# Performance work log

Measured on AMD Instinct MI355X. Metric: run time of the kernel, lower is better.

Reference implementation:

```python
import jax, jax.numpy as jnp
import numpy as np

S, D_MODEL, D_INTERNAL = 4096, 2048, 512


def setup_inputs() -> dict:
    key = jax.random.key(0)
    ks = jax.random.split(key, 11)
    sc_in = 1.0 / np.sqrt(D_MODEL)
    return {
        "input_vecs": jax.random.normal(ks[0], (S, D_MODEL), jnp.float32),
        "qw": jax.random.normal(ks[1], (D_INTERNAL, D_MODEL), jnp.float32) * sc_in,
        "qb": jax.random.normal(ks[2], (D_INTERNAL,), jnp.float32) * 0.01,
        "kw": jax.random.normal(ks[3], (D_INTERNAL, D_MODEL), jnp.float32) * sc_in,
        "kb": jax.random.normal(ks[4], (D_INTERNAL,), jnp.float32) * 0.01,
        "vw": jax.random.normal(ks[5], (D_MODEL, D_MODEL), jnp.float32) * sc_in,
        "vb": jax.random.normal(ks[6], (D_MODEL,), jnp.float32) * 0.01,
        "w1": jax.random.normal(ks[7], (D_MODEL, D_MODEL), jnp.float32) * sc_in,
        "b1": jax.random.normal(ks[8], (D_MODEL,), jnp.float32) * 0.01,
        "w2": jax.random.normal(ks[9], (D_MODEL, D_MODEL), jnp.float32) * sc_in,
        "b2": jax.random.normal(ks[10], (D_MODEL,), jnp.float32) * 0.01,
    }


def reference(input_vecs, qw, qb, kw, kb, vw, vb, w1, b1, w2, b2):
    # torch nn.Linear: y = x @ W.T + b
    q = input_vecs @ qw.T + qb              # [S, d_internal]
    k = input_vecs @ kw.T + kb              # [S, d_internal]
    v = input_vecs @ vw.T + vb              # [S, d_model]
    scale = 1.0 / jnp.sqrt(jnp.float32(D_INTERNAL))
    attn = jax.nn.softmax((q @ k.T) * scale, axis=-1)  # [S, S]
    h = attn @ v                            # [S, d_model]
    x_residual = h + input_vecs
    x = jax.nn.relu(x_residual @ w1.T + b1)
    x = x @ w2.T + b2
    hidden = x + x_residual
    return hidden, k, v
```

## Files before the change

kernel.cpp:

```cpp
#include <hip/hip_runtime.h>
#include <cstdint>
#include <cstddef>


typedef __attribute__((ext_vector_type(8))) short short8;
typedef __attribute__((ext_vector_type(4))) float f32x4;

typedef __attribute__((address_space(3))) void lds_void;
typedef __attribute__((address_space(1))) void g_void;

#define SEQ    4096
#define DMODEL 2048
#define DINT   512

#define MEMF() asm volatile("" ::: "memory")
#define BARRIER() do { MEMF(); __builtin_amdgcn_s_barrier(); MEMF(); } while (0)
#define VMCNT6() asm volatile("s_waitcnt vmcnt(6)" ::: "memory")
#define VMCNT0() asm volatile("s_waitcnt vmcnt(0)" ::: "memory")
#define LGKM0()  asm volatile("s_waitcnt lgkmcnt(0)" ::: "memory")

__device__ __forceinline__ unsigned short f2bf(float f) {
  union { float f; unsigned int u; } a;
  a.f = f;
  unsigned int u = a.u;
  u += 0x7fffu + ((u >> 16) & 1u);
  return (unsigned short)(u >> 16);
}

__global__ __launch_bounds__(256) void cast_bf16_kernel(
    const float* __restrict__ in, unsigned short* __restrict__ out, int n4) {
  int i = blockIdx.x * 256 + threadIdx.x;
  if (i >= n4) return;
  float4 v = ((const float4*)in)[i];
  ushort4 o;
  o.x = f2bf(v.x); o.y = f2bf(v.y); o.z = f2bf(v.z); o.w = f2bf(v.w);
  ((ushort4*)out)[i] = o;
}

__global__ __launch_bounds__(256) void transpose_bf16_kernel(
    const unsigned short* __restrict__ in, unsigned short* __restrict__ out,
    int R, int C) {
  __shared__ unsigned short tile[64][65];
  const int tx = threadIdx.x & 63;
  const int ty = threadIdx.x >> 6;
  const int r0 = blockIdx.x * 64;
  const int c0 = blockIdx.y * 64;
#pragma unroll
  for (int i = 0; i < 64; i += 4)
    tile[ty + i][tx] = in[(size_t)(r0 + ty + i) * C + c0 + tx];
  __syncthreads();
#pragma unroll
  for (int i = 0; i < 64; i += 4)
    out[(size_t)(c0 + ty + i) * R + r0 + tx] = tile[tx][ty + i];
}

__global__ __launch_bounds__(256)
void gemm_qkv_kernel(const unsigned short* __restrict__ A,
                     const unsigned short* __restrict__ W,
                     int M, int N, int K,
                     const float* __restrict__ qb,
                     const float* __restrict__ kb,
                     const float* __restrict__ vb,
                     float* __restrict__ outK,
                     float* __restrict__ outV,
                     unsigned short* __restrict__ Qb,
                     unsigned short* __restrict__ Kb,
                     unsigned short* __restrict__ Vb)
{
  __shared__ __align__(16) unsigned short As[2][128][32];
  __shared__ __align__(16) unsigned short Bs[2][128][32];

  const int tid  = threadIdx.x;
  const int lane = tid & 63;
  const int wave = tid >> 6;
  const int wr   = wave >> 1;
  const int wc   = wave & 1;
  const int brow = blockIdx.x * 128;
  const int bcol = blockIdx.y * 128;
  const int lr   = lane & 15;
  const int kg   = lane >> 4;

  const int srow  = tid >> 2;
  const int scol  = (tid & 3) * 8;
  const int wbase = wave * 16;
  const unsigned short* Ab = A + (size_t)(brow + srow) * K + scol;
  const unsigned short* Bb = W + (size_t)(bcol + srow) * K + scol;

  f32x4 acc[4][4];
#pragma unroll
  for (int i = 0; i < 4; i++)
#pragma unroll
    for (int j = 0; j < 4; j++) acc[i][j] = (f32x4){0.f, 0.f, 0.f, 0.f};

  auto stage = [&](int d, int k0) {
#pragma unroll
    for (int j = 0; j < 2; ++j) {
      __builtin_amdgcn_global_load_lds((const g_void*)(Ab + (size_t)(j * 64) * K + k0),
                                       (lds_void*)&As[d][j * 64 + wbase][0], 16, 0, 0);
      __builtin_amdgcn_global_load_lds((const g_void*)(Bb + (size_t)(j * 64) * K + k0),
                                       (lds_void*)&Bs[d][j * 64 + wbase][0], 16, 0, 0);
    }
  };

  auto compute = [&](int d) {
    short8 aF[4], bF[4];
#pragma unroll
    for (int mi = 0; mi < 4; ++mi)
      aF[mi] = *(const short8*)&As[d][wr * 64 + mi * 16 + lr][kg * 8];
#pragma unroll
    for (int ni = 0; ni < 4; ++ni)
      bF[ni] = *(const short8*)&Bs[d][wc * 64 + ni * 16 + lr][kg * 8];
#pragma unroll
    for (int mi = 0; mi < 4; ++mi)
#pragma unroll
      for (int ni = 0; ni < 4; ++ni)
        acc[mi][ni] = __builtin_amdgcn_mfma_f32_16x16x32_bf16(
            aF[mi], bF[ni], acc[mi][ni], 0, 0, 0);
  };

  stage(0, 0);
  __syncthreads();
  int c = 0;
  const int NT = K >> 5;
  for (int t = 0; t < NT; ++t) {
    if (t + 1 < NT) stage(c ^ 1, (t + 1) << 5);
    compute(c);
    __syncthreads();
    c ^= 1;
  }

#pragma unroll
  for (int mi = 0; mi < 4; mi++) {
#pragma unroll
    for (int ni = 0; ni < 4; ni++) {
#pragma unroll
      for (int r = 0; r < 4; r++) {
        const int row = brow + wr * 64 + mi * 16 + kg * 4 + r;
        const int col = bcol + wc * 64 + ni * 16 + lr;
        float v = acc[mi][ni][r];
        if (col < 512) {
          v += qb[col];
          Qb[(size_t)row * 512 + col] = f2bf(v);
        } else if (col < 1024) {
          const int c2 = col - 512;
          v += kb[c2];
          outK[(size_t)row * 512 + c2] = v;
          Kb[(size_t)row * 512 + c2] = f2bf(v);
        } else {
          const int c2 = col - 1024;
          v += vb[c2];
          outV[(size_t)row * 2048 + c2] = v;
          Vb[(size_t)row * 2048 + c2] = f2bf(v);
        }
      }
    }
  }
}

__global__ __launch_bounds__(512, 2)
void gemm256_kernel(const unsigned short* __restrict__ A,
                    const unsigned short* __restrict__ B,
                    int M, int N, int K,
                    const float* __restrict__ bias,
                    const float* __restrict__ resid,
                    float scale, int relu,
                    float* __restrict__ outF,
                    unsigned short* __restrict__ outB)
{
  __shared__ __align__(16) unsigned short lds[2][2][2][128][64];

  const int tid  = threadIdx.x;
  const int lane = tid & 63;
  const int wave = tid >> 6;
  const int wm   = wave >> 2;
  const int wn   = wave & 3;
  const int lr   = lane & 15;
  const int kg   = lane >> 4;
  const int brow = blockIdx.x * 256;
  const int bcol = blockIdx.y * 256;

  const int srow = tid >> 3;
  const int ssw  = ((tid & 7) * 8) ^ ((srow & 7) << 3);
  const unsigned short* Asrc = A + (size_t)(brow + srow) * K + ssw;
  const unsigned short* Bsrc = B + (size_t)(bcol + srow) * K + ssw;

  char* lbase = (char*)&lds[0][0][0][0][0];
  const int woff = wave * 1024;

  f32x4 acc[8][4];
#pragma unroll
  for (int i = 0; i < 8; ++i)
#pragma unroll
    for (int j = 0; j < 4; ++j) acc[i][j] = (f32x4){0.f, 0.f, 0.f, 0.f};

  const int NT = K >> 6;

  auto SA = [&](int d, int h, int q, int tl) {
    __builtin_amdgcn_global_load_lds(
        (const g_void*)(Asrc + (size_t)(h * 128 + q * 64) * K + tl * 64),
        (lds_void*)(lbase + d * 32768 + h * 16384 + q * 8192 + woff), 16, 0, 0);
  };
  auto SB = [&](int d, int h, int q, int tl) {
    __builtin_amdgcn_global_load_lds(
        (const g_void*)(Bsrc + (size_t)(h * 128 + q * 64) * K + tl * 64),
        (lds_void*)(lbase + 65536 + d * 32768 + h * 16384 + q * 8192 + woff), 16, 0, 0);
  };

  auto LDA = [&](short8* a, int d, int mh, int ks) {
    const char* reg = lbase + d * 32768 + wm * 16384;
    const int ke = (ks * 32 + kg * 8) ^ ((lr & 7) << 3);
#pragma unroll
    for (int i = 0; i < 4; ++i) {
      const int row = (mh * 4 + i) * 16 + lr;
      a[i] = *(const short8*)(reg + row * 128 + ke * 2);
    }
  };
  auto LDB = [&](short8* b, int d, int ks) {
    const char* reg = lbase + 65536 + d * 32768 + (wn >> 1) * 16384;
    const int ke = (ks * 32 + kg * 8) ^ ((lr & 7) << 3);
#pragma unroll
    for (int n = 0; n < 4; ++n) {
      const int row = (wn & 1) * 64 + n * 16 + lr;
      b[n] = *(const short8*)(reg + row * 128 + ke * 2);
    }
  };

  auto MM = [&](int mh, short8* a, short8* b) {
    __builtin_amdgcn_s_setprio(1);
#pragma unroll
    for (int i = 0; i < 4; ++i)
#pragma unroll
      for (int n = 0; n < 4; ++n)
        acc[mh * 4 + i][n] = __builtin_amdgcn_mfma_f32_16x16x32_bf16(
            a[i], b[n], acc[mh * 4 + i][n], 0, 0, 0);
    __builtin_amdgcn_s_setprio(0);
  };

  SA(0, 0, 0, 0); SA(0, 0, 1, 0); SA(0, 1, 0, 0); SA(0, 1, 1, 0);
  SB(0, 0, 0, 0); SB(0, 0, 1, 0); SB(0, 1, 0, 0); SB(0, 1, 1, 0);
  SB(1, 0, 0, 1); SB(1, 0, 1, 1); SA(1, 0, 0, 1);
  SB(1, 1, 0, 1); SB(1, 1, 1, 1); SA(1, 1, 0, 1);
  VMCNT6();
  BARRIER();

  short8 aT[4], bF0[4], bF1[4];
  for (int t = 0; t < NT; ++t) {
    const int buf = t & 1, nb = buf ^ 1;
    const int t1 = (t + 1 < NT) ? t + 1 : NT - 1;
    const int t2 = (t + 2 < NT) ? t + 2 : NT - 1;

    LDA(aT, buf, 0, 0); LDB(bF0, buf, 0);
    SA(nb, 0, 1, t1); SA(nb, 1, 1, t1);
    BARRIER(); MM(0, aT, bF0); BARRIER();

    LDA(aT, buf, 0, 1); LDB(bF1, buf, 1);
    BARRIER(); MM(0, aT, bF1); BARRIER();

    LDA(aT, buf, 1, 0);
    SB(buf, 0, 0, t2); SB(buf, 0, 1, t2); SA(buf, 0, 0, t2);
    BARRIER(); MM(1, aT, bF0); BARRIER();

    LDA(aT, buf, 1, 1);
    SB(buf, 1, 0, t2); SB(buf, 1, 1, t2); SA(buf, 1, 0, t2);
    BARRIER(); MM(1, aT, bF1);
    VMCNT6();
    BARRIER();
  }
  VMCNT0();

#pragma unroll
  for (int mi = 0; mi < 8; ++mi) {
#pragma unroll
    for (int ni = 0; ni < 4; ++ni) {
#pragma unroll
      for (int r = 0; r < 4; ++r) {
        const int row = brow + wm * 128 + mi * 16 + kg * 4 + r;
        const int col = bcol + wn * 64 + ni * 16 + lr;
        float v = acc[mi][ni][r] * scale;
        if (bias)  v += bias[col];
        if (resid) v += resid[(size_t)row * N + col];
        if (relu)  v = fmaxf(v, 0.0f);
        if (outF)  outF[(size_t)row * N + col] = v;
        if (outB)  outB[(size_t)row * N + col] = f2bf(v);
      }
    }
  }
}

__global__ __launch_bounds__(512, 2)
void gemm256x128_kernel(const unsigned short* __restrict__ A,
                        const unsigned short* __restrict__ B,
                        int M, int N, int K,
                        const float* __restrict__ bias,
                        const float* __restrict__ resid,
                        float scale, int relu,
                        float* __restrict__ outF,
                        unsigned short* __restrict__ outB)
{
  __shared__ __align__(16) unsigned short lds[49152];

  const int tid  = threadIdx.x;
  const int lane = tid & 63;
  const int wave = tid >> 6;
  const int wm   = wave >> 1;
  const int wn   = wave & 1;
  const int lr   = lane & 15;
  const int kg   = lane >> 4;
  const int brow = blockIdx.x * 256;
  const int bcol = blockIdx.y * 128;

  const int srow = tid >> 3;
  const int ssw  = ((tid & 7) * 8) ^ ((srow & 7) << 3);
  const unsigned short* Asrc = A + (size_t)(brow + srow) * K + ssw;
  const unsigned short* Bsrc = B + (size_t)(bcol + srow) * K + ssw;

  char* lbase = (char*)&lds[0];
  const int woff = wave * 1024;

  f32x4 acc[4][4];
#pragma unroll
  for (int i = 0; i < 4; ++i)
#pragma unroll
    for (int j = 0; j < 4; ++j) acc[i][j] = (f32x4){0.f, 0.f, 0.f, 0.f};

  const int NT = K >> 6;

  auto STAGE = [&](int d, int tl) {
#pragma unroll
    for (int r = 0; r < 4; ++r)
      __builtin_amdgcn_global_load_lds(
          (const g_void*)(Asrc + (size_t)(r * 64) * K + tl * 64),
          (lds_void*)(lbase + d * 32768 + r * 8192 + woff), 16, 0, 0);
#pragma unroll
    for (int r = 0; r < 2; ++r)
      __builtin_amdgcn_global_load_lds(
          (const g_void*)(Bsrc + (size_t)(r * 64) * K + tl * 64),
          (lds_void*)(lbase + 65536 + d * 16384 + r * 8192 + woff), 16, 0, 0);
  };

  auto RD = [&](short8* a, short8* b, int d) {
#pragma unroll
    for (int ks = 0; ks < 2; ++ks) {
      const int ke = (ks * 32 + kg * 8) ^ ((lr & 7) << 3);
      const char* ra = lbase + d * 32768;
      const char* rb = lbase + 65536 + d * 16384;
#pragma unroll
      for (int mi = 0; mi < 4; ++mi)
        a[ks * 4 + mi] = *(const short8*)(ra + (wm * 64 + mi * 16 + lr) * 128 + ke * 2);
#pragma unroll
      for (int n = 0; n < 4; ++n)
        b[ks * 4 + n] = *(const short8*)(rb + (wn * 64 + n * 16 + lr) * 128 + ke * 2);
    }
  };

  auto MMALL = [&](short8* a, short8* b) {
    __builtin_amdgcn_s_setprio(1);
#pragma unroll
    for (int ks = 0; ks < 2; ++ks)
#pragma unroll
      for (int mi = 0; mi < 4; ++mi)
#pragma unroll
        for (int n = 0; n < 4; ++n)
          acc[mi][n] = __builtin_amdgcn_mfma_f32_16x16x32_bf16(
              a[ks * 4 + mi], b[ks * 4 + n], acc[mi][n], 0, 0, 0);
    __builtin_amdgcn_s_setprio(0);
  };

  STAGE(0, 0);
  STAGE(1, 1);
  VMCNT0();
  BARRIER();
  short8 aE[8], bE[8], aO[8], bO[8];
  RD(aE, bE, 0);
  LGKM0();

  for (int t = 0; t < NT; t += 2) {
    VMCNT0();
    BARRIER();
    { const int t2 = (t + 2 < NT) ? t + 2 : NT - 1; STAGE(0, t2); }
    RD(aO, bO, 1);
    MMALL(aE, bE);
    LGKM0();
    VMCNT0();
    BARRIER();
    { const int t3 = (t + 3 < NT) ? t + 3 : NT - 1; STAGE(1, t3); }
    RD(aE, bE, 0);
    MMALL(aO, bO);
    LGKM0();
  }
  VMCNT0();

#pragma unroll
  for (int mi = 0; mi < 4; ++mi) {
#pragma unroll
    for (int ni = 0; ni < 4; ++ni) {
#pragma unroll
      for (int r = 0; r < 4; ++r) {
        const int row = brow + wm * 64 + mi * 16 + kg * 4 + r;
        const int col = bcol + wn * 64 + ni * 16 + lr;
        float v = acc[mi][ni][r] * scale;
        if (bias)  v += bias[col];
        if (resid) v += resid[(size_t)row * N + col];
        if (relu)  v = fmaxf(v, 0.0f);
        if (outF)  outF[(size_t)row * N + col] = v;
        if (outB)  outB[(size_t)row * N + col] = f2bf(v);
      }
    }
  }
}

__global__ __launch_bounds__(256) void softmax_kernel(
    const float* __restrict__ Sc, unsigned short* __restrict__ P) {
  __shared__ float redm[4];
  __shared__ float reds[4];
  const int tid = threadIdx.x;
  const int row = blockIdx.x;
  const float* src = Sc + (size_t)row * SEQ;

  float4 f0 = *(const float4*)(src + tid * 4);
  float4 f1 = *(const float4*)(src + tid * 4 + 1024);
  float4 f2 = *(const float4*)(src + tid * 4 + 2048);
  float4 f3 = *(const float4*)(src + tid * 4 + 3072);

  float lmax = fmaxf(fmaxf(fmaxf(f0.x, f0.y), fmaxf(f0.z, f0.w)),
                     fmaxf(fmaxf(f1.x, f1.y), fmaxf(f1.z, f1.w)));
  lmax = fmaxf(lmax, fmaxf(fmaxf(f2.x, f2.y), fmaxf(f2.z, f2.w)));
  lmax = fmaxf(lmax, fmaxf(fmaxf(f3.x, f3.y), fmaxf(f3.z, f3.w)));
#pragma unroll
  for (int off = 32; off > 0; off >>= 1)
    lmax = fmaxf(lmax, __shfl_xor(lmax, off, 64));
  if ((tid & 63) == 0) redm[tid >> 6] = lmax;
  __syncthreads();
  const float m = fmaxf(fmaxf(redm[0], redm[1]), fmaxf(redm[2], redm[3]));

  f0.x = __expf(f0.x - m); f0.y = __expf(f0.y - m);
  f0.z = __expf(f0.z - m); f0.w = __expf(f0.w - m);
  f1.x = __expf(f1.x - m); f1.y = __expf(f1.y - m);
  f1.z = __expf(f1.z - m); f1.w = __expf(f1.w - m);
  f2.x = __expf(f2.x - m); f2.y = __expf(f2.y - m);
  f2.z = __expf(f2.z - m); f2.w = __expf(f2.w - m);
  f3.x = __expf(f3.x - m); f3.y = __expf(f3.y - m);
  f3.z = __expf(f3.z - m); f3.w = __expf(f3.w - m);

  float lsum = (f0.x + f0.y + f0.z + f0.w) + (f1.x + f1.y + f1.z + f1.w) +
               (f2.x + f2.y + f2.z + f2.w) + (f3.x + f3.y + f3.z + f3.w);
#pragma unroll
  for (int off = 32; off > 0; off >>= 1)
    lsum += __shfl_xor(lsum, off, 64);
  if ((tid & 63) == 0) reds[tid >> 6] = lsum;
  __syncthreads();
  const float inv = 1.0f / (reds[0] + reds[1] + reds[2] + reds[3]);

  unsigned short* dst = P + (size_t)row * SEQ;
  ushort4 o0 = { f2bf(f0.x * inv), f2bf(f0.y * inv), f2bf(f0.z * inv), f2bf(f0.w * inv) };
  ushort4 o1 = { f2bf(f1.x * inv), f2bf(f1.y * inv), f2bf(f1.z * inv), f2bf(f1.w * inv) };
  ushort4 o2 = { f2bf(f2.x * inv), f2bf(f2.y * inv), f2bf(f2.z * inv), f2bf(f2.w * inv) };
  ushort4 o3 = { f2bf(f3.x * inv), f2bf(f3.y * inv), f2bf(f3.z * inv), f2bf(f3.w * inv) };
  *(ushort4*)(dst + tid * 4)        = o0;
  *(ushort4*)(dst + tid * 4 + 1024) = o1;
  *(ushort4*)(dst + tid * 4 + 2048) = o2;
  *(ushort4*)(dst + tid * 4 + 3072) = o3;
}

extern "C" void kernel_launch(void* const* d_in, const int* in_sizes, int n_in,
                              void* d_out, int out_size, void* d_ws, size_t ws_size,
                              hipStream_t stream) {
  const float* x  = (const float*)d_in[0];
  const float* qw = (const float*)d_in[1];
  const float* qb = (const float*)d_in[2];
  const float* kw = (const float*)d_in[3];
  const float* kb = (const float*)d_in[4];
  const float* vw = (const float*)d_in[5];
  const float* vb = (const float*)d_in[6];
  const float* w1 = (const float*)d_in[7];
  const float* b1 = (const float*)d_in[8];
  const float* w2 = (const float*)d_in[9];
  const float* b2 = (const float*)d_in[10];
  float* out = (float*)d_out;
  char* ws = (char*)d_ws;

  const size_t MB = 1048576;
  unsigned short* Xb    = (unsigned short*)(ws + 0 * MB);
  unsigned short* QKVWb = (unsigned short*)(ws + 16 * MB);
  unsigned short* Pb    = (unsigned short*)(ws + 0 * MB);
  unsigned short* W1b   = (unsigned short*)(ws + 32 * MB);
  unsigned short* W2b   = (unsigned short*)(ws + 40 * MB);
  unsigned short* Qb    = (unsigned short*)(ws + 48 * MB);
  unsigned short* Kb    = (unsigned short*)(ws + 52 * MB);
  unsigned short* Vb    = (unsigned short*)(ws + 56 * MB);
  unsigned short* VTb   = (unsigned short*)(ws + 72 * MB);
  float*          Sc    = (float*)(ws + 88 * MB);
  float*          XR    = (float*)(ws + 88 * MB);
  unsigned short* X1b   = (unsigned short*)(ws + 120 * MB);
  unsigned short* XRb   = (unsigned short*)(ws + 136 * MB);

  cast_bf16_kernel<<<8192, 256, 0, stream>>>(x,  Xb, 2097152);
  cast_bf16_kernel<<<1024, 256, 0, stream>>>(qw, QKVWb, 262144);
  cast_bf16_kernel<<<1024, 256, 0, stream>>>(kw, QKVWb + 512 * 2048, 262144);
  cast_bf16_kernel<<<4096, 256, 0, stream>>>(vw, QKVWb + 1024 * 2048, 1048576);
  cast_bf16_kernel<<<4096, 256, 0, stream>>>(w1, W1b, 1048576);
  cast_bf16_kernel<<<4096, 256, 0, stream>>>(w2, W2b, 1048576);

  gemm_qkv_kernel<<<dim3(32, 24), dim3(256), 0, stream>>>(
      Xb, QKVWb, SEQ, 3072, DMODEL, qb, kb, vb,
      out + 8388608, out + 10485760, Qb, Kb, Vb);
  transpose_bf16_kernel<<<dim3(64, 32), dim3(256), 0, stream>>>(Vb, VTb, SEQ, DMODEL);
  gemm256_kernel<<<dim3(16, 16), dim3(512), 0, stream>>>(
      Qb, Kb, SEQ, SEQ, DINT, nullptr, nullptr,
      0.04419417382415922f, 0, Sc, nullptr);
  softmax_kernel<<<4096, dim3(256), 0, stream>>>(Sc, Pb);
  gemm256x128_kernel<<<dim3(16, 16), dim3(512), 0, stream>>>(
      Pb, VTb, SEQ, DMODEL, SEQ, nullptr, x, 1.0f, 0, XR, XRb);
  gemm256x128_kernel<<<dim3(16, 16), dim3(512), 0, stream>>>(
      XRb, W1b, SEQ, DMODEL, DMODEL, b1, nullptr, 1.0f, 1, nullptr, X1b);
  gemm256x128_kernel<<<dim3(16, 16), dim3(512), 0, stream>>>(
      X1b, W2b, SEQ, DMODEL, DMODEL, b2, XR, 1.0f, 0, out, nullptr);
}
```

Before: 359.4 us.

## Merge casts, fuse V transpose, store bf16 scores, triple-buffer GEMM pipeline

The six fp32-to-bf16 cast launches become one kernel. The QKV GEMM epilogue now writes V directly in transposed bf16 layout, so the separate transpose kernel is gone. The QK^T score matrix is stored as bf16 instead of fp32, which halves score traffic into softmax but rounds the logits before exponentiation. The 256x128 GEMM moves from double to triple LDS buffering with partial vmcnt waits, using more LDS per block, which may limit occupancy with two blocks per CU.

```diff
diff --git a/kernel.cpp b/kernel.cpp
--- a/kernel.cpp
+++ b/kernel.cpp
@@ -15,6 +15,7 @@
 
 #define MEMF() asm volatile("" ::: "memory")
 #define BARRIER() do { MEMF(); __builtin_amdgcn_s_barrier(); MEMF(); } while (0)
+#define VMCNT12() asm volatile("s_waitcnt vmcnt(12)" ::: "memory")
 #define VMCNT6() asm volatile("s_waitcnt vmcnt(6)" ::: "memory")
 #define VMCNT0() asm volatile("s_waitcnt vmcnt(0)" ::: "memory")
 #define LGKM0()  asm volatile("s_waitcnt lgkmcnt(0)" ::: "memory")
@@ -26,32 +27,30 @@
   u += 0x7fffu + ((u >> 16) & 1u);
   return (unsigned short)(u >> 16);
 }
-
-__global__ __launch_bounds__(256) void cast_bf16_kernel(
-    const float* __restrict__ in, unsigned short* __restrict__ out, int n4) {
-  int i = blockIdx.x * 256 + threadIdx.x;
-  if (i >= n4) return;
-  float4 v = ((const float4*)in)[i];
+__device__ __forceinline__ float bf2f(unsigned short u) {
+  union { unsigned int i; float f; } a;
+  a.i = ((unsigned int)u) << 16;
+  return a.f;
+}
+
+__global__ __launch_bounds__(256) void cast_all_kernel(
+    const float* __restrict__ x,  const float* __restrict__ qw,
+    const float* __restrict__ kw, const float* __restrict__ vw,
+    const float* __restrict__ w1, const float* __restrict__ w2,
+    unsigned short* __restrict__ Xb, unsigned short* __restrict__ QKVWb,
+    unsigned short* __restrict__ W1b, unsigned short* __restrict__ W2b) {
+  const int i = blockIdx.x * 256 + threadIdx.x;
+  const float* src; unsigned short* dst; int off;
+  if (i < 2097152)      { src = x;  dst = Xb;               off = i; }
+  else if (i < 2359296) { src = qw; dst = QKVWb;            off = i - 2097152; }
+  else if (i < 2621440) { src = kw; dst = QKVWb + 1048576;  off = i - 2359296; }
+  else if (i < 3670016) { src = vw; dst = QKVWb + 2097152;  off = i - 2621440; }
+  else if (i < 4718592) { src = w1; dst = W1b;              off = i - 3670016; }
+  else                  { src = w2; dst = W2b;              off = i - 4718592; }
+  float4 v = ((const float4*)src)[off];
   ushort4 o;
   o.x = f2bf(v.x); o.y = f2bf(v.y); o.z = f2bf(v.z); o.w = f2bf(v.w);
-  ((ushort4*)out)[i] = o;
-}
-
-__global__ __launch_bounds__(256) void transpose_bf16_kernel(
-    const unsigned short* __restrict__ in, unsigned short* __restrict__ out,
-    int R, int C) {
-  __shared__ unsigned short tile[64][65];
-  const int tx = threadIdx.x & 63;
-  const int ty = threadIdx.x >> 6;
-  const int r0 = blockIdx.x * 64;
-  const int c0 = blockIdx.y * 64;
-#pragma unroll
-  for (int i = 0; i < 64; i += 4)
-    tile[ty + i][tx] = in[(size_t)(r0 + ty + i) * C + c0 + tx];
-  __syncthreads();
-#pragma unroll
-  for (int i = 0; i < 64; i += 4)
-    out[(size_t)(c0 + ty + i) * R + r0 + tx] = tile[tx][ty + i];
+  ((ushort4*)dst)[off] = o;
 }
 
 __global__ __launch_bounds__(256)
@@ -65,7 +64,7 @@
                      float* __restrict__ outV,
                      unsigned short* __restrict__ Qb,
                      unsigned short* __restrict__ Kb,
-                     unsigned short* __restrict__ Vb)
+                     unsigned short* __restrict__ VTb)
 {
   __shared__ __align__(16) unsigned short As[2][128][32];
   __shared__ __align__(16) unsigned short Bs[2][128][32];
@@ -133,25 +132,33 @@
   for (int mi = 0; mi < 4; mi++) {
 #pragma unroll
     for (int ni = 0; ni < 4; ni++) {
-#pragma unroll
-      for (int r = 0; r < 4; r++) {
-        const int row = brow + wr * 64 + mi * 16 + kg * 4 + r;
-        const int col = bcol + wc * 64 + ni * 16 + lr;
-        float v = acc[mi][ni][r];
-        if (col < 512) {
-          v += qb[col];
-          Qb[(size_t)row * 512 + col] = f2bf(v);
-        } else if (col < 1024) {
-          const int c2 = col - 512;
-          v += kb[c2];
-          outK[(size_t)row * 512 + c2] = v;
-          Kb[(size_t)row * 512 + c2] = f2bf(v);
-        } else {
-          const int c2 = col - 1024;
-          v += vb[c2];
-          outV[(size_t)row * 2048 + c2] = v;
-          Vb[(size_t)row * 2048 + c2] = f2bf(v);
+      const int row0 = brow + wr * 64 + mi * 16 + kg * 4;
+      const int col  = bcol + wc * 64 + ni * 16 + lr;
+      if (col < 512) {
+        const float b = qb[col];
+#pragma unroll
+        for (int r = 0; r < 4; r++)
+          Qb[(size_t)(row0 + r) * 512 + col] = f2bf(acc[mi][ni][r] + b);
+      } else if (col < 1024) {
+        const int c2 = col - 512;
+        const float b = kb[c2];
+#pragma unroll
+        for (int r = 0; r < 4; r++) {
+          const float t = acc[mi][ni][r] + b;
+          outK[(size_t)(row0 + r) * 512 + c2] = t;
+          Kb[(size_t)(row0 + r) * 512 + c2] = f2bf(t);
         }
+      } else {
+        const int c2 = col - 1024;
+        const float b = vb[c2];
+        ushort4 o;
+#pragma unroll
+        for (int r = 0; r < 4; r++) {
+          const float t = acc[mi][ni][r] + b;
+          outV[(size_t)(row0 + r) * 2048 + c2] = t;
+          ((unsigned short*)&o)[r] = f2bf(t);
+        }
+        *(ushort4*)(&VTb[(size_t)c2 * 4096 + row0]) = o;
       }
     }
   }
@@ -288,16 +295,16 @@
 }
 
 __global__ __launch_bounds__(512, 2)
-void gemm256x128_kernel(const unsigned short* __restrict__ A,
-                        const unsigned short* __restrict__ B,
-                        int M, int N, int K,
-                        const float* __restrict__ bias,
-                        const float* __restrict__ resid,
-                        float scale, int relu,
-                        float* __restrict__ outF,
-                        unsigned short* __restrict__ outB)
+void gemm256x128_k3_kernel(const unsigned short* __restrict__ A,
+                           const unsigned short* __restrict__ B,
+                           int M, int N, int K,
+                           const float* __restrict__ bias,
+                           const float* __restrict__ resid,
+                           float scale, int relu,
+                           float* __restrict__ outF,
+                           unsigned short* __restrict__ outB)
 {
-  __shared__ __align__(16) unsigned short lds[49152];
+  __shared__ __align__(16) unsigned short lds[73728];
 
   const int tid  = threadIdx.x;
   const int lane = tid & 63;
@@ -335,7 +342,7 @@
     for (int r = 0; r < 2; ++r)
       __builtin_amdgcn_global_load_lds(
           (const g_void*)(Bsrc + (size_t)(r * 64) * K + tl * 64),
-          (lds_void*)(lbase + 65536 + d * 16384 + r * 8192 + woff), 16, 0, 0);
+          (lds_void*)(lbase + 98304 + d * 16384 + r * 8192 + woff), 16, 0, 0);
   };
 
   auto RD = [&](short8* a, short8* b, int d) {
@@ -343,7 +350,7 @@
     for (int ks = 0; ks < 2; ++ks) {
       const int ke = (ks * 32 + kg * 8) ^ ((lr & 7) << 3);
       const char* ra = lbase + d * 32768;
-      const char* rb = lbase + 65536 + d * 16384;
+      const char* rb = lbase + 98304 + d * 16384;
 #pragma unroll
       for (int mi = 0; mi < 4; ++mi)
         a[ks * 4 + mi] = *(const short8*)(ra + (wm * 64 + mi * 16 + lr) * 128 + ke * 2);
@@ -368,23 +375,24 @@
 
   STAGE(0, 0);
   STAGE(1, 1);
-  VMCNT0();
+  STAGE(2, 2);
+  VMCNT12();
   BARRIER();
   short8 aE[8], bE[8], aO[8], bO[8];
   RD(aE, bE, 0);
   LGKM0();
 
   for (int t = 0; t < NT; t += 2) {
-    VMCNT0();
+    VMCNT6();
     BARRIER();
-    { const int t2 = (t + 2 < NT) ? t + 2 : NT - 1; STAGE(0, t2); }
-    RD(aO, bO, 1);
+    STAGE(t % 3, (t + 3 < NT) ? t + 3 : NT - 1);
+    RD(aO, bO, (t + 1) % 3);
     MMALL(aE, bE);
     LGKM0();
-    VMCNT0();
+    VMCNT6();
     BARRIER();
-    { const int t3 = (t + 3 < NT) ? t + 3 : NT - 1; STAGE(1, t3); }
-    RD(aE, bE, 0);
+    STAGE((t + 1) % 3, (t + 4 < NT) ? t + 4 : NT - 1);
+    RD(aE, bE, (t + 2) % 3);
     MMALL(aO, bO);
     LGKM0();
   }
@@ -410,22 +418,24 @@
 }
 
 __global__ __launch_bounds__(256) void softmax_kernel(
-    const float* __restrict__ Sc, unsigned short* __restrict__ P) {
+    const unsigned short* __restrict__ Scb, unsigned short* __restrict__ P) {
   __shared__ float redm[4];
   __shared__ float reds[4];
   const int tid = threadIdx.x;
   const int row = blockIdx.x;
-  const float* src = Sc + (size_t)row * SEQ;
-
-  float4 f0 = *(const float4*)(src + tid * 4);
-  float4 f1 = *(const float4*)(src + tid * 4 + 1024);
-  float4 f2 = *(const float4*)(src + tid * 4 + 2048);
-  float4 f3 = *(const float4*)(src + tid * 4 + 3072);
-
-  float lmax = fmaxf(fmaxf(fmaxf(f0.x, f0.y), fmaxf(f0.z, f0.w)),
-                     fmaxf(fmaxf(f1.x, f1.y), fmaxf(f1.z, f1.w)));
-  lmax = fmaxf(lmax, fmaxf(fmaxf(f2.x, f2.y), fmaxf(f2.z, f2.w)));
-  lmax = fmaxf(lmax, fmaxf(fmaxf(f3.x, f3.y), fmaxf(f3.z, f3.w)));
+  const unsigned short* src = Scb + (size_t)row * SEQ;
+
+  short8 h0 = *(const short8*)(src + tid * 8);
+  short8 h1 = *(const short8*)(src + tid * 8 + 2048);
+  float f[16];
+#pragma unroll
+  for (int i = 0; i < 8; ++i) f[i]     = bf2f((unsigned short)h0[i]);
+#pragma unroll
+  for (int i = 0; i < 8; ++i) f[8 + i] = bf2f((unsigned short)h1[i]);
+
+  float lmax = f[0];
+#pragma unroll
+  for (int i = 1; i < 16; ++i) lmax = fmaxf(lmax, f[i]);
 #pragma unroll
   for (int off = 32; off > 0; off >>= 1)
     lmax = fmaxf(lmax, __shfl_xor(lmax, off, 64));
@@ -433,17 +443,9 @@
   __syncthreads();
   const float m = fmaxf(fmaxf(redm[0], redm[1]), fmaxf(redm[2], redm[3]));
 
-  f0.x = __expf(f0.x - m); f0.y = __expf(f0.y - m);
-  f0.z = __expf(f0.z - m); f0.w = __expf(f0.w - m);
-  f1.x = __expf(f1.x - m); f1.y = __expf(f1.y - m);
-  f1.z = __expf(f1.z - m); f1.w = __expf(f1.w - m);
-  f2.x = __expf(f2.x - m); f2.y = __expf(f2.y - m);
-  f2.z = __expf(f2.z - m); f2.w = __expf(f2.w - m);
-  f3.x = __expf(f3.x - m); f3.y = __expf(f3.y - m);
-  f3.z = __expf(f3.z - m); f3.w = __expf(f3.w - m);
-
-  float lsum = (f0.x + f0.y + f0.z + f0.w) + (f1.x + f1.y + f1.z + f1.w) +
-               (f2.x + f2.y + f2.z + f2.w) + (f3.x + f3.y + f3.z + f3.w);
+  float lsum = 0.0f;
+#pragma unroll
+  for (int i = 0; i < 16; ++i) { f[i] = __expf(f[i] - m); lsum += f[i]; }
 #pragma unroll
   for (int off = 32; off > 0; off >>= 1)
     lsum += __shfl_xor(lsum, off, 64);
@@ -452,14 +454,13 @@
   const float inv = 1.0f / (reds[0] + reds[1] + reds[2] + reds[3]);
 
   unsigned short* dst = P + (size_t)row * SEQ;
-  ushort4 o0 = { f2bf(f0.x * inv), f2bf(f0.y * inv), f2bf(f0.z * inv), f2bf(f0.w * inv) };
-  ushort4 o1 = { f2bf(f1.x * inv), f2bf(f1.y * inv), f2bf(f1.z * inv), f2bf(f1.w * inv) };
-  ushort4 o2 = { f2bf(f2.x * inv), f2bf(f2.y * inv), f2bf(f2.z * inv), f2bf(f2.w * inv) };
-  ushort4 o3 = { f2bf(f3.x * inv), f2bf(f3.y * inv), f2bf(f3.z * inv), f2bf(f3.w * inv) };
-  *(ushort4*)(dst + tid * 4)        = o0;
-  *(ushort4*)(dst + tid * 4 + 1024) = o1;
-  *(ushort4*)(dst + tid * 4 + 2048) = o2;
-  *(ushort4*)(dst + tid * 4 + 3072) = o3;
+  short8 o0, o1;
+#pragma unroll
+  for (int i = 0; i < 8; ++i) o0[i] = (short)f2bf(f[i] * inv);
+#pragma unroll
+  for (int i = 0; i < 8; ++i) o1[i] = (short)f2bf(f[8 + i] * inv);
+  *(short8*)(dst + tid * 8)        = o0;
+  *(short8*)(dst + tid * 8 + 2048) = o1;
 }
 
 extern "C" void kernel_launch(void* const* d_in, const int* in_sizes, int n_in,
@@ -487,32 +488,26 @@
   unsigned short* W2b   = (unsigned short*)(ws + 40 * MB);
   unsigned short* Qb    = (unsigned short*)(ws + 48 * MB);
   unsigned short* Kb    = (unsigned short*)(ws + 52 * MB);
-  unsigned short* Vb    = (unsigned short*)(ws + 56 * MB);
   unsigned short* VTb   = (unsigned short*)(ws + 72 * MB);
-  float*          Sc    = (float*)(ws + 88 * MB);
+  unsigned short* Scb   = (unsigned short*)(ws + 88 * MB);
   float*          XR    = (float*)(ws + 88 * MB);
   unsigned short* X1b   = (unsigned short*)(ws + 120 * MB);
   unsigned short* XRb   = (unsigned short*)(ws + 136 * MB);
 
-  cast_bf16_kernel<<<8192, 256, 0, stream>>>(x,  Xb, 2097152);
-  cast_bf16_kernel<<<1024, 256, 0, stream>>>(qw, QKVWb, 262144);
-  cast_bf16_kernel<<<1024, 256, 0, stream>>>(kw, QKVWb + 512 * 2048, 262144);
-  cast_bf16_kernel<<<4096, 256, 0, stream>>>(vw, QKVWb + 1024 * 2048, 1048576);
-  cast_bf16_kernel<<<4096, 256, 0, stream>>>(w1, W1b, 1048576);
-  cast_bf16_kernel<<<4096, 256, 0, stream>>>(w2, W2b, 1048576);
+  cast_all_kernel<<<22528, 256, 0, stream>>>(
+      x, qw, kw, vw, w1, w2, Xb, QKVWb, W1b, W2b);
 
   gemm_qkv_kernel<<<dim3(32, 24), dim3(256), 0, stream>>>(
       Xb, QKVWb, SEQ, 3072, DMODEL, qb, kb, vb,
-      out + 8388608, out + 10485760, Qb, Kb, Vb);
-  transpose_bf16_kernel<<<dim3(64, 32), dim3(256), 0, stream>>>(Vb, VTb, SEQ, DMODEL);
+      out + 8388608, out + 10485760, Qb, Kb, VTb);
   gemm256_kernel<<<dim3(16, 16), dim3(512), 0, stream>>>(
       Qb, Kb, SEQ, SEQ, DINT, nullptr, nullptr,
-      0.04419417382415922f, 0, Sc, nullptr);
-  softmax_kernel<<<4096, dim3(256), 0, stream>>>(Sc, Pb);
-  gemm256x128_kernel<<<dim3(16, 16), dim3(512), 0, stream>>>(
+      0.04419417382415922f, 0, nullptr, Scb);
+  softmax_kernel<<<4096, dim3(256), 0, stream>>>(Scb, Pb);
+  gemm256x128_k3_kernel<<<dim3(16, 16), dim3(512), 0, stream>>>(
       Pb, VTb, SEQ, DMODEL, SEQ, nullptr, x, 1.0f, 0, XR, XRb);
-  gemm256x128_kernel<<<dim3(16, 16), dim3(512), 0, stream>>>(
+  gemm256x128_k3_kernel<<<dim3(16, 16), dim3(512), 0, stream>>>(
       XRb, W1b, SEQ, DMODEL, DMODEL, b1, nullptr, 1.0f, 1, nullptr, X1b);
-  gemm256x128_kernel<<<dim3(16, 16), dim3(512), 0, stream>>>(
+  gemm256x128_k3_kernel<<<dim3(16, 16), dim3(512), 0, stream>>>(
       X1b, W2b, SEQ, DMODEL, DMODEL, b2, XR, 1.0f, 0, out, nullptr);
 }
```

Result: faster. 325.5 us (-9.4%).
